# Performance work log

Measured on AMD Instinct MI355X. Metric: run time of the kernel, lower is better.

## Reference

```python
import jax, jax.numpy as jnp
import numpy as np

B, NT, NW, D, H = 32768, 10, 3, 64, 4
EPS = 1e-5

def _ln(x, g, b):
    mu = jnp.mean(x, axis=-1, keepdims=True)
    var = jnp.mean((x - mu) ** 2, axis=-1, keepdims=True)
    return (x - mu) * jax.lax.rsqrt(var + EPS) * g + b

def _mha(q_in, kv, wq, bq, wk, bk, wv, bv, wo, bo):
    Bb, Lq, Dm = q_in.shape
    Lk = kv.shape[1]
    dh = Dm // H
    q = (q_in @ wq + bq).reshape(Bb, Lq, H, dh)
    k = (kv @ wk + bk).reshape(Bb, Lk, H, dh)
    v = (kv @ wv + bv).reshape(Bb, Lk, H, dh)
    s = jnp.einsum('bqhd,bkhd->bhqk', q, k) / np.float32(np.sqrt(dh))
    a = jax.nn.softmax(s, axis=-1)
    o = jnp.einsum('bhqk,bkhd->bqhd', a, v).reshape(Bb, Lq, Dm)
    return o @ wo + bo

def setup_inputs() -> dict:
    key = jax.random.key(0)
    ks = iter(jax.random.split(key, 40))
    def rn(shape, scale=0.05):
        return jax.random.normal(next(ks), shape, dtype=jnp.float32) * scale
    inp = {
        'track_left': jax.random.normal(next(ks), (B, NT, 2), dtype=jnp.float32),
        'track_right': jax.random.normal(next(ks), (B, NT, 2), dtype=jnp.float32),
        'qemb': rn((NW, D), 1.0),
        'ip_w1': rn((2, D // 2)), 'ip_b1': jnp.zeros((D // 2,), jnp.float32),
        'ip_w2': rn((D // 2, D)), 'ip_b2': jnp.zeros((D,), jnp.float32),
    }
    for p in ('a1', 'a2'):
        for nm in ('wq', 'wk', 'wv', 'wo'):
            inp[p + '_' + nm] = rn((D, D))
        for nm in ('bq', 'bk', 'bv', 'bo'):
            inp[p + '_' + nm] = jnp.zeros((D,), jnp.float32)
    inp['ffn_w1'] = rn((D, 2 * D)); inp['ffn_b1'] = jnp.zeros((2 * D,), jnp.float32)
    inp['ffn_w2'] = rn((2 * D, D)); inp['ffn_b2'] = jnp.zeros((D,), jnp.float32)
    for n in ('n1', 'n2', 'n3'):
        inp[n + '_g'] = jnp.ones((D,), jnp.float32)
        inp[n + '_b'] = jnp.zeros((D,), jnp.float32)
    inp['op_w1'] = rn((D, D // 2)); inp['op_b1'] = jnp.zeros((D // 2,), jnp.float32)
    inp['op_w2'] = rn((D // 2, 2)); inp['op_b2'] = jnp.zeros((2,), jnp.float32)
    return inp

def reference(track_left, track_right, qemb, ip_w1, ip_b1, ip_w2, ip_b2,
              a1_wq, a1_bq, a1_wk, a1_bk, a1_wv, a1_bv, a1_wo, a1_bo,
              a2_wq, a2_bq, a2_wk, a2_bk, a2_wv, a2_bv, a2_wo, a2_bo,
              ffn_w1, ffn_b1, ffn_w2, ffn_b2,
              n1_g, n1_b, n2_g, n2_b, n3_g, n3_b,
              op_w1, op_b1, op_w2, op_b2):
    # concat left/right boundaries -> [B, 2*NT, 2]
    pts = jnp.concatenate([track_left, track_right], axis=1)
    # input projection MLP -> [B, 2*NT, D]
    feats = jax.nn.relu(pts @ ip_w1 + ip_b1) @ ip_w2 + ip_b2
    # learned waypoint queries broadcast over batch -> [B, NW, D]
    q0 = jnp.broadcast_to(qemb[None], (pts.shape[0], NW, D))
    x1 = _ln(q0 + _mha(q0, feats, a1_wq, a1_bq, a1_wk, a1_bk, a1_wv, a1_bv, a1_wo, a1_bo), n1_g, n1_b)
    x2 = _ln(x1 + _mha(x1, feats, a2_wq, a2_bq, a2_wk, a2_bk, a2_wv, a2_bv, a2_wo, a2_bo), n2_g, n2_b)
    f = jax.nn.relu(x2 @ ffn_w1 + ffn_b1) @ ffn_w2 + ffn_b2
    x3 = _ln(x2 + f, n3_g, n3_b)
    # output projection -> [B, NW, 2]
    return jax.nn.relu(x3 @ op_w1 + op_b1) @ op_w2 + op_b2
```

## Files before the change

kernel.cpp:

```cpp
#include <hip/hip_runtime.h>
#include <math.h>

#define SCALE 0.36067376022224085f

#define WVF1F 0
#define WVF2F 2048
#define WKT2F 4096
#define G1F   6144
#define BVF1F 6528
#define BVF2F 6592

#define WSYNC() do { asm volatile("s_waitcnt lgkmcnt(0)" ::: "memory"); __builtin_amdgcn_wave_barrier(); } while (0)

struct Params {
  const float* tl; const float* tr; const float* qemb;
  const float* ip_w1; const float* ip_b1;
  const float* wq2; const float* bq2;
  const float* wo1; const float* bo1;
  const float* wo2; const float* bo2;
  const float* ffn_w1; const float* ffn_b1;
  const float* ffn_w2; const float* ffn_b2;
  const float* n1_g; const float* n1_b;
  const float* n2_g; const float* n2_b;
  const float* n3_g; const float* n3_b;
  const float* op_w1; const float* op_b1;
  const float* op_w2; const float* op_b2;
  const float* ws;
  float* out;
};

__global__ void prep1_kernel(const float* ip_w2, const float* ip_b2,
                             const float* wk2, const float* wv1, const float* wv2,
                             const float* bv1, const float* bv2, float* ws) {
  const int bid = blockIdx.x, tid = threadIdx.x;
  if (bid < 24) {
    const int idx = bid * 256 + tid;
    const int mat = idx >> 11;
    const int rem = idx & 2047;
    const int j = rem >> 6, c = rem & 63;
    const float* W = (mat == 0) ? wv1 : (mat == 1) ? wv2 : wk2;
    float acc = 0.f;
    for (int m = 0; m < 64; ++m) acc = fmaf(ip_w2[j * 64 + m], W[m * 64 + c], acc);
    if (mat == 0)      ws[WVF1F + j * 64 + c] = acc;
    else if (mat == 1) ws[WVF2F + j * 64 + c] = acc;
    else               ws[WKT2F + c * 32 + j] = acc * SCALE;
  } else if (tid < 128) {
    const int l = tid >> 6, d = tid & 63;
    const float* bv = l ? bv2 : bv1;
    const float* wv = l ? wv2 : wv1;
    float acc = bv[d];
    for (int m = 0; m < 64; ++m) acc = fmaf(ip_b2[m], wv[m * 64 + d], acc);
    ws[(l ? BVF2F : BVF1F) + d] = acc;
  }
}

__global__ void prep2_kernel(const float* ip_w2, const float* wk1,
                             const float* qemb, const float* wq1, const float* bq1,
                             float* ws) {
  __shared__ float wkf[32][64];
  __shared__ float q1[3][64];
  const int tid = threadIdx.x;
  for (int e = tid; e < 2048; e += 384) {
    const int j = e >> 6, c = e & 63;
    float acc = 0.f;
    for (int m = 0; m < 64; ++m) acc = fmaf(ip_w2[j * 64 + m], wk1[m * 64 + c], acc);
    wkf[j][c] = acc;
  }
  if (tid < 192) {
    const int q = tid >> 6, d = tid & 63;
    float acc = bq1[d];
    for (int e = 0; e < 64; ++e) acc = fmaf(qemb[q * 64 + e], wq1[e * 64 + d], acc);
    q1[q][d] = acc;
  }
  __syncthreads();
  {
    const int r = tid >> 5, j = tid & 31;
    const int h = r / 3, q = r - h * 3;
    float acc = 0.f;
    for (int d = 0; d < 16; ++d) acc = fmaf(wkf[j][h * 16 + d], q1[q][h * 16 + d], acc);
    ws[G1F + r * 32 + j] = acc * SCALE;
  }
}

__global__ __launch_bounds__(256) void planner_kernel(Params p) {
  const int w = threadIdx.x >> 6;
  const int lane = threadIdx.x & 63;
  const int item = blockIdx.x * 4 + w;

  __shared__ __align__(16) float g1_s[12][36];
  __shared__ __align__(16) float a_s[4][20][36];
  __shared__ __align__(16) float att_s[4][12][24];
  __shared__ __align__(16) float ch_s[4][12][36];
  __shared__ __align__(16) float qx_s[4][3][68];
  __shared__ __align__(16) float x_s[4][3][68];
  __shared__ float pts_s[4][40];

  const float* ws = p.ws;

  for (int e = threadIdx.x; e < 384; e += 256)
    g1_s[e >> 5][e & 31] = ws[G1F + e];

  if (lane < 40)
    pts_s[w][lane] = (lane < 20) ? p.tl[item * 20 + lane] : p.tr[item * 20 + lane - 20];
  WSYNC();

  {
    const int j = lane & 31, th = lane >> 5;
    const float w0 = p.ip_w1[j], w1 = p.ip_w1[32 + j], b = p.ip_b1[j];
#pragma unroll
    for (int i = 0; i < 10; ++i) {
      const int t = th * 10 + i;
      a_s[w][t][j] = fmaxf(fmaf(pts_s[w][2 * t], w0, fmaf(pts_s[w][2 * t + 1], w1, b)), 0.f);
    }
  }
  __syncthreads();

  const int t3 = lane / 3;
  const int q3 = lane - t3 * 3;
  const int j32 = lane & 31, half = lane >> 5, hq0 = half * 6;
  const int h16 = lane >> 4;

  float xq[3];

#pragma unroll
  for (int l = 0; l < 2; ++l) {
    if (l == 1) {
      float acc[3];
#pragma unroll
      for (int q = 0; q < 3; ++q) acc[q] = p.bq2[lane];
#pragma unroll
      for (int jc = 0; jc < 16; ++jc) {
        float wv[4];
#pragma unroll
        for (int r = 0; r < 4; ++r) wv[r] = p.wq2[(jc * 4 + r) * 64 + lane];
#pragma unroll
        for (int q = 0; q < 3; ++q) {
          const float4 xv = *(const float4*)&x_s[w][q][jc * 4];
          acc[q] = fmaf(xv.x, wv[0], fmaf(xv.y, wv[1], fmaf(xv.z, wv[2], fmaf(xv.w, wv[3], acc[q]))));
        }
      }
#pragma unroll
      for (int q = 0; q < 3; ++q) qx_s[w][q][lane] = acc[q];
      WSYNC();
      {
        float g2[6] = {0, 0, 0, 0, 0, 0};
        const int D0 = half * 32;
#pragma unroll
        for (int dd = 0; dd < 32; ++dd) {
          const int D = D0 + dd;
          const float wk = ws[WKT2F + D * 32 + j32];
          const int hl = dd >> 4;
#pragma unroll
          for (int q = 0; q < 3; ++q)
            g2[hl * 3 + q] = fmaf(wk, qx_s[w][q][D], g2[hl * 3 + q]);
        }
#pragma unroll
        for (int k = 0; k < 6; ++k) ch_s[w][hq0 + k][j32] = g2[k];
      }
      WSYNC();
    }

    const float (*g)[36] = (l == 0) ? (const float (*)[36])g1_s : (const float (*)[36])ch_s[w];
    if (lane < 60) {
      float acc[4] = {0, 0, 0, 0};
#pragma unroll
      for (int jc = 0; jc < 8; ++jc) {
        const float4 av = *(const float4*)&a_s[w][t3][jc * 4];
#pragma unroll
        for (int h = 0; h < 4; ++h) {
          const float4 gv = *(const float4*)&g[h * 3 + q3][jc * 4];
          acc[h] = fmaf(av.x, gv.x, fmaf(av.y, gv.y, fmaf(av.z, gv.z, fmaf(av.w, gv.w, acc[h]))));
        }
      }
#pragma unroll
      for (int h = 0; h < 4; ++h) att_s[w][h * 3 + q3][t3] = acc[h];
    }
    WSYNC();

    if (lane < 12) {
      float m = -1e30f;
#pragma unroll
      for (int t = 0; t < 20; ++t) m = fmaxf(m, att_s[w][lane][t]);
      float s = 0.f;
#pragma unroll
      for (int t = 0; t < 20; ++t) {
        const float e = exp2f(att_s[w][lane][t] - m);
        att_s[w][lane][t] = e;
        s += e;
      }
      att_s[w][lane][20] = 1.f / s;
    }
    WSYNC();

    {
      float c[6] = {0, 0, 0, 0, 0, 0};
#pragma unroll
      for (int tc = 0; tc < 5; ++tc) {
        float av[4];
#pragma unroll
        for (int r = 0; r < 4; ++r) av[r] = a_s[w][tc * 4 + r][j32];
#pragma unroll
        for (int k = 0; k < 6; ++k) {
          const float4 at = *(const float4*)&att_s[w][hq0 + k][tc * 4];
          c[k] = fmaf(at.x, av[0], fmaf(at.y, av[1], fmaf(at.z, av[2], fmaf(at.w, av[3], c[k]))));
        }
      }
#pragma unroll
      for (int k = 0; k < 6; ++k)
        ch_s[w][hq0 + k][j32] = c[k] * att_s[w][hq0 + k][20];
    }
    WSYNC();

    {
      const float* Wv = ws + (l ? WVF2F : WVF1F);
      const float bv = ws[(l ? BVF2F : BVF1F) + lane];
      float o[3] = {bv, bv, bv};
#pragma unroll
      for (int jc = 0; jc < 8; ++jc) {
        float wv[4];
#pragma unroll
        for (int r = 0; r < 4; ++r) wv[r] = Wv[(jc * 4 + r) * 64 + lane];
#pragma unroll
        for (int q = 0; q < 3; ++q) {
          const float4 cv = *(const float4*)&ch_s[w][h16 * 3 + q][jc * 4];
          o[q] = fmaf(cv.x, wv[0], fmaf(cv.y, wv[1], fmaf(cv.z, wv[2], fmaf(cv.w, wv[3], o[q]))));
        }
      }
#pragma unroll
      for (int q = 0; q < 3; ++q) qx_s[w][q][lane] = o[q];
    }
    WSYNC();

    {
      const float* wo = l ? p.wo2 : p.wo1;
      const float* bo = l ? p.bo2 : p.bo1;
      const float* gg = l ? p.n2_g : p.n1_g;
      const float* gb = l ? p.n2_b : p.n1_b;
      float acc[3];
#pragma unroll
      for (int q = 0; q < 3; ++q)
        acc[q] = bo[lane] + (l ? x_s[w][q][lane] : p.qemb[q * 64 + lane]);
#pragma unroll
      for (int jc = 0; jc < 16; ++jc) {
        float wv[4];
#pragma unroll
        for (int r = 0; r < 4; ++r) wv[r] = wo[(jc * 4 + r) * 64 + lane];
#pragma unroll
        for (int q = 0; q < 3; ++q) {
          const float4 ov = *(const float4*)&qx_s[w][q][jc * 4];
          acc[q] = fmaf(ov.x, wv[0], fmaf(ov.y, wv[1], fmaf(ov.z, wv[2], fmaf(ov.w, wv[3], acc[q]))));
        }
      }
      const float gv = gg[lane], bv = gb[lane];
#pragma unroll
      for (int q = 0; q < 3; ++q) {
        const float v = acc[q];
        float s = v;
#pragma unroll
        for (int m = 32; m >= 1; m >>= 1) s += __shfl_xor(s, m);
        const float mu = s * (1.f / 64.f);
        const float d = v - mu;
        float s2 = d * d;
#pragma unroll
        for (int m = 32; m >= 1; m >>= 1) s2 += __shfl_xor(s2, m);
        const float inv = rsqrtf(s2 * (1.f / 64.f) + 1e-5f);
        const float xn = fmaf(d * inv, gv, bv);
        xq[q] = xn;
        x_s[w][q][lane] = xn;
      }
    }
    WSYNC();
  }

  float* f1p = (float*)a_s[w];
  {
    float a0[3], a1[3];
    const float b0 = p.ffn_b1[lane], b1 = p.ffn_b1[64 + lane];
#pragma unroll
    for (int q = 0; q < 3; ++q) { a0[q] = b0; a1[q] = b1; }
#pragma unroll
    for (int jc = 0; jc < 16; ++jc) {
      float w0[4], w1[4];
#pragma unroll
      for (int r = 0; r < 4; ++r) {
        w0[r] = p.ffn_w1[(jc * 4 + r) * 128 + lane];
        w1[r] = p.ffn_w1[(jc * 4 + r) * 128 + 64 + lane];
      }
#pragma unroll
      for (int q = 0; q < 3; ++q) {
        const float4 xv = *(const float4*)&x_s[w][q][jc * 4];
        a0[q] = fmaf(xv.x, w0[0], fmaf(xv.y, w0[1], fmaf(xv.z, w0[2], fmaf(xv.w, w0[3], a0[q]))));
        a1[q] = fmaf(xv.x, w1[0], fmaf(xv.y, w1[1], fmaf(xv.z, w1[2], fmaf(xv.w, w1[3], a1[q]))));
      }
    }
#pragma unroll
    for (int q = 0; q < 3; ++q) {
      f1p[q * 136 + lane] = fmaxf(a0[q], 0.f);
      f1p[q * 136 + 64 + lane] = fmaxf(a1[q], 0.f);
    }
  }
  WSYNC();

  {
    float acc[3];
#pragma unroll
    for (int q = 0; q < 3; ++q) acc[q] = p.ffn_b2[lane] + xq[q];
#pragma unroll
    for (int mc = 0; mc < 32; ++mc) {
      float wv[4];
#pragma unroll
      for (int r = 0; r < 4; ++r) wv[r] = p.ffn_w2[(mc * 4 + r) * 64 + lane];
#pragma unroll
      for (int q = 0; q < 3; ++q) {
        const float4 fv = *(const float4*)&f1p[q * 136 + mc * 4];
        acc[q] = fmaf(fv.x, wv[0], fmaf(fv.y, wv[1], fmaf(fv.z, wv[2], fmaf(fv.w, wv[3], acc[q]))));
      }
    }
    const float gv = p.n3_g[lane], bv = p.n3_b[lane];
#pragma unroll
    for (int q = 0; q < 3; ++q) {
      const float v = acc[q];
      float s = v;
#pragma unroll
      for (int m = 32; m >= 1; m >>= 1) s += __shfl_xor(s, m);
      const float mu = s * (1.f / 64.f);
      const float d = v - mu;
      float s2 = d * d;
#pragma unroll
      for (int m = 32; m >= 1; m >>= 1) s2 += __shfl_xor(s2, m);
      const float inv = rsqrtf(s2 * (1.f / 64.f) + 1e-5f);
      x_s[w][q][lane] = fmaf(d * inv, gv, bv);
    }
  }
  WSYNC();

  if (lane < 32) {
    float acc[3];
#pragma unroll
    for (int q = 0; q < 3; ++q) acc[q] = p.op_b1[lane];
#pragma unroll
    for (int jc = 0; jc < 16; ++jc) {
      float wv[4];
#pragma unroll
      for (int r = 0; r < 4; ++r) wv[r] = p.op_w1[(jc * 4 + r) * 32 + lane];
#pragma unroll
      for (int q = 0; q < 3; ++q) {
        const float4 xv = *(const float4*)&x_s[w][q][jc * 4];
        acc[q] = fmaf(xv.x, wv[0], fmaf(xv.y, wv[1], fmaf(xv.z, wv[2], fmaf(xv.w, wv[3], acc[q]))));
      }
    }
#pragma unroll
    for (int q = 0; q < 3; ++q) qx_s[w][q][lane] = fmaxf(acc[q], 0.f);
  }
  WSYNC();

  if (lane < 6) {
    const int q = lane >> 1, e = lane & 1;
    float acc = p.op_b2[e];
#pragma unroll
    for (int m = 0; m < 32; ++m) acc = fmaf(qx_s[w][q][m], p.op_w2[m * 2 + e], acc);
    p.out[item * 6 + q * 2 + e] = acc;
  }
}

extern "C" void kernel_launch(void* const* d_in, const int* in_sizes, int n_in,
                              void* d_out, int out_size, void* d_ws, size_t ws_size,
                              hipStream_t stream) {
  const float* in[40];
  for (int i = 0; i < n_in && i < 40; ++i) in[i] = (const float*)d_in[i];

  const float *a1_wq, *a1_wk, *a1_wv, *a1_wo, *a1_bq, *a1_bk, *a1_bv, *a1_bo;
  const float *a2_wq, *a2_wk, *a2_wv, *a2_wo, *a2_bq, *a2_bk, *a2_bv, *a2_bo;
  if (in_sizes[8] == 4096) {
    a1_wq = in[7];  a1_wk = in[8];  a1_wv = in[9];  a1_wo = in[10];
    a1_bq = in[11]; a1_bk = in[12]; a1_bv = in[13]; a1_bo = in[14];
    a2_wq = in[15]; a2_wk = in[16]; a2_wv = in[17]; a2_wo = in[18];
    a2_bq = in[19]; a2_bk = in[20]; a2_bv = in[21]; a2_bo = in[22];
  } else {
    a1_wq = in[7];  a1_bq = in[8];  a1_wk = in[9];  a1_bk = in[10];
    a1_wv = in[11]; a1_bv = in[12]; a1_wo = in[13]; a1_bo = in[14];
    a2_wq = in[15]; a2_bq = in[16]; a2_wk = in[17]; a2_bk = in[18];
    a2_wv = in[19]; a2_bv = in[20]; a2_wo = in[21]; a2_bo = in[22];
  }
  (void)a1_bk; (void)a2_bk;

  float* ws = (float*)d_ws;
  prep1_kernel<<<25, 256, 0, stream>>>(in[5], in[6], a2_wk, a1_wv, a2_wv, a1_bv, a2_bv, ws);
  prep2_kernel<<<1, 384, 0, stream>>>(in[5], a1_wk, in[2], a1_wq, a1_bq, ws);

  Params p;
  p.tl = in[0]; p.tr = in[1]; p.qemb = in[2];
  p.ip_w1 = in[3]; p.ip_b1 = in[4];
  p.wq2 = a2_wq; p.bq2 = a2_bq;
  p.wo1 = a1_wo; p.bo1 = a1_bo;
  p.wo2 = a2_wo; p.bo2 = a2_bo;
  p.ffn_w1 = in[23]; p.ffn_b1 = in[24]; p.ffn_w2 = in[25]; p.ffn_b2 = in[26];
  p.n1_g = in[27]; p.n1_b = in[28]; p.n2_g = in[29]; p.n2_b = in[30];
  p.n3_g = in[31]; p.n3_b = in[32];
  p.op_w1 = in[33]; p.op_b1 = in[34]; p.op_w2 = in[35]; p.op_b2 = in[36];
  p.ws = ws; p.out = (float*)d_out;

  planner_kernel<<<8192, 256, 0, stream>>>(p);
}
```

Baseline: 258.1 us.

## Rewrite planner kernel around split-bf16 MFMA with two items per wave

Replaces the scalar FMA matrix products with 16x16x32 bf16 MFMA instructions, using a three-term hi/lo bf16 split to approximate fp32 accuracy. Weights are pre-split and pre-swizzled into fragment layout by new prep kernels, and each wave now processes two batch items, so the grid is halved. Small parameters are staged in shared memory. The aim is to cut VALU work per item; the cost is extra conversion work, larger LDS use that may reduce occupancy, and a small loss of precision.

```diff
diff --git a/kernel.cpp b/kernel.cpp
--- a/kernel.cpp
+++ b/kernel.cpp
@@ -3,363 +3,571 @@
 
 #define SCALE 0.36067376022224085f
 
-#define WVF1F 0
-#define WVF2F 2048
-#define WKT2F 4096
-#define G1F   6144
-#define BVF1F 6528
-#define BVF2F 6592
+typedef __attribute__((ext_vector_type(8))) short short8;
+typedef __attribute__((ext_vector_type(4))) float f32x4;
+
+#define G1H 0
+#define G1L 512
+#define WV1H 1024
+#define WV1L 3072
+#define WV2H 5120
+#define WV2L 7168
+#define WKT2H 9216
+#define WKT2L 11264
+#define WQ2H 13312
+#define WQ2L 17408
+#define WO1H 21504
+#define WO1L 25600
+#define WO2H 29696
+#define WO2L 33792
+#define F1H 37888
+#define F1L 46080
+#define F2H 54272
+#define F2L 62464
+#define OP1H 70656
+#define OP1L 72704
+#define WKF1T 37376
+#define WKF2T 39424
+#define WVF1T 41472
+#define WVF2T 43520
+#define Q1T   45568
+#define BV1T  45760
 
 #define WSYNC() do { asm volatile("s_waitcnt lgkmcnt(0)" ::: "memory"); __builtin_amdgcn_wave_barrier(); } while (0)
 
+__device__ __forceinline__ unsigned short f2bf(float x) {
+  unsigned u = __builtin_bit_cast(unsigned, x);
+  return (unsigned short)((u + 0x7fffu + ((u >> 16) & 1u)) >> 16);
+}
+__device__ __forceinline__ float bf2f(unsigned short h) {
+  unsigned u = ((unsigned)h) << 16;
+  return __builtin_bit_cast(float, u);
+}
+__device__ __forceinline__ void lds_frag(const float* row, int koff, short8& fh, short8& fl) {
+  const float4 a = *(const float4*)(row + koff);
+  const float4 b = *(const float4*)(row + koff + 4);
+  float v[8] = {a.x, a.y, a.z, a.w, b.x, b.y, b.z, b.w};
+#pragma unroll
+  for (int j = 0; j < 8; ++j) {
+    unsigned short h = f2bf(v[j]);
+    fh[j] = (short)h;
+    fl[j] = (short)f2bf(v[j] - bf2f(h));
+  }
+}
+__device__ __forceinline__ short8 ldg_frag(const unsigned short* base, int idx) {
+  return __builtin_bit_cast(short8, *(const float4*)(base + idx));
+}
+#define MFMA3(acc, ah, al, bh, bl)                                      \
+  acc = __builtin_amdgcn_mfma_f32_16x16x32_bf16(ah, bh, acc, 0, 0, 0);  \
+  acc = __builtin_amdgcn_mfma_f32_16x16x32_bf16(ah, bl, acc, 0, 0, 0);  \
+  acc = __builtin_amdgcn_mfma_f32_16x16x32_bf16(al, bh, acc, 0, 0, 0);
+
 struct Params {
-  const float* tl; const float* tr; const float* qemb;
-  const float* ip_w1; const float* ip_b1;
-  const float* wq2; const float* bq2;
-  const float* wo1; const float* bo1;
-  const float* wo2; const float* bo2;
-  const float* ffn_w1; const float* ffn_b1;
-  const float* ffn_w2; const float* ffn_b2;
-  const float* n1_g; const float* n1_b;
-  const float* n2_g; const float* n2_b;
-  const float* n3_g; const float* n3_b;
-  const float* op_w1; const float* op_b1;
-  const float* op_w2; const float* op_b2;
-  const float* ws;
+  const float *tl, *tr, *qemb, *ip_w1, *ip_b1;
+  const float *bq2, *bo1, *bo2, *fb1, *fb2, *opb1, *opw2, *opb2;
+  const float *n1g, *n1b, *n2g, *n2b, *n3g, *n3b;
+  const float* wsf;
+  const unsigned short* wsb;
   float* out;
 };
 
-__global__ void prep1_kernel(const float* ip_w2, const float* ip_b2,
-                             const float* wk2, const float* wv1, const float* wv2,
-                             const float* bv1, const float* bv2, float* ws) {
+__global__ void prepA_kernel(const float* ip_w2, const float* ip_b2,
+                             const float* wk1, const float* wk2,
+                             const float* wv1, const float* wv2,
+                             const float* bv1, const float* bv2,
+                             const float* qemb, const float* wq1, const float* bq1,
+                             float* wsf) {
   const int bid = blockIdx.x, tid = threadIdx.x;
-  if (bid < 24) {
-    const int idx = bid * 256 + tid;
-    const int mat = idx >> 11;
-    const int rem = idx & 2047;
+  if (bid < 32) {
+    const int e = bid * 256 + tid;
+    const int mat = e >> 11, rem = e & 2047;
     const int j = rem >> 6, c = rem & 63;
-    const float* W = (mat == 0) ? wv1 : (mat == 1) ? wv2 : wk2;
+    const float* W = (mat == 0) ? wk1 : (mat == 1) ? wk2 : (mat == 2) ? wv1 : wv2;
     float acc = 0.f;
     for (int m = 0; m < 64; ++m) acc = fmaf(ip_w2[j * 64 + m], W[m * 64 + c], acc);
-    if (mat == 0)      ws[WVF1F + j * 64 + c] = acc;
-    else if (mat == 1) ws[WVF2F + j * 64 + c] = acc;
-    else               ws[WKT2F + c * 32 + j] = acc * SCALE;
-  } else if (tid < 128) {
-    const int l = tid >> 6, d = tid & 63;
-    const float* bv = l ? bv2 : bv1;
-    const float* wv = l ? wv2 : wv1;
-    float acc = bv[d];
-    for (int m = 0; m < 64; ++m) acc = fmaf(ip_b2[m], wv[m * 64 + d], acc);
-    ws[(l ? BVF2F : BVF1F) + d] = acc;
-  }
-}
-
-__global__ void prep2_kernel(const float* ip_w2, const float* wk1,
-                             const float* qemb, const float* wq1, const float* bq1,
-                             float* ws) {
-  __shared__ float wkf[32][64];
-  __shared__ float q1[3][64];
-  const int tid = threadIdx.x;
-  for (int e = tid; e < 2048; e += 384) {
-    const int j = e >> 6, c = e & 63;
-    float acc = 0.f;
-    for (int m = 0; m < 64; ++m) acc = fmaf(ip_w2[j * 64 + m], wk1[m * 64 + c], acc);
-    wkf[j][c] = acc;
-  }
-  if (tid < 192) {
-    const int q = tid >> 6, d = tid & 63;
-    float acc = bq1[d];
-    for (int e = 0; e < 64; ++e) acc = fmaf(qemb[q * 64 + e], wq1[e * 64 + d], acc);
-    q1[q][d] = acc;
+    wsf[WKF1T + e] = acc;
+  } else if (bid == 32) {
+    if (tid < 192) {
+      const int q = tid >> 6, d = tid & 63;
+      float acc = bq1[d];
+      for (int e = 0; e < 64; ++e) acc = fmaf(qemb[q * 64 + e], wq1[e * 64 + d], acc);
+      wsf[Q1T + tid] = acc;
+    }
+  } else {
+    if (tid < 128) {
+      const int lyr = tid >> 6, d = tid & 63;
+      const float* bv = lyr ? bv2 : bv1;
+      const float* wv = lyr ? wv2 : wv1;
+      float acc = bv[d];
+      for (int m = 0; m < 64; ++m) acc = fmaf(ip_b2[m], wv[m * 64 + d], acc);
+      wsf[BV1T + tid] = acc;
+    }
+  }
+}
+
+__global__ void prepB_kernel(float* wsf, unsigned short* wsb,
+                             const float* wq2, const float* wo1, const float* wo2,
+                             const float* fw1, const float* fw2, const float* opw1) {
+  const int bid = blockIdx.x, tid = threadIdx.x;
+  if (bid == 0) {
+    __shared__ float g1f[32][16];
+    {
+      const int j = tid >> 4, col = tid & 15;
+      float acc = 0.f;
+      if (col < 12) {
+        const int h = (col * 11) >> 5, q = col - 3 * h;
+        for (int d = 0; d < 16; ++d)
+          acc = fmaf(wsf[WKF1T + j * 64 + h * 16 + d], wsf[Q1T + q * 64 + h * 16 + d], acc);
+        acc *= SCALE;
+      }
+      g1f[j][col] = acc;
+    }
+    __syncthreads();
+    {
+      const int e = tid, j8 = e & 7, ln = (e >> 3) & 63;
+      const int k = (ln >> 4) * 8 + j8, n = ln & 15;
+      const float val = g1f[k][n];
+      const unsigned short h = f2bf(val);
+      wsb[G1H + e] = h;
+      wsb[G1L + e] = f2bf(val - bf2f(h));
+    }
+    return;
+  }
+  const int pe = (bid - 1) * 512 + tid;
+  const int j8 = pe & 7, ln = (pe >> 3) & 63;
+  const int krow = (ln >> 4) * 8 + j8, ncol = ln & 15;
+  float val;
+  int hOff, lOff, loc;
+  if (pe < 2048) {
+    loc = pe; const int nt = (loc >> 9) & 3;
+    val = wsf[WVF1T + krow * 64 + nt * 16 + ncol];
+    hOff = WV1H; lOff = WV1L;
+  } else if (pe < 4096) {
+    loc = pe - 2048; const int nt = (loc >> 9) & 3;
+    val = wsf[WVF2T + krow * 64 + nt * 16 + ncol];
+    hOff = WV2H; lOff = WV2L;
+  } else if (pe < 6144) {
+    loc = pe - 4096; const int nt = (loc >> 9) & 1, kt = (loc >> 10) & 1;
+    val = SCALE * wsf[WKF2T + (nt * 16 + ncol) * 64 + kt * 32 + krow];
+    hOff = WKT2H; lOff = WKT2L;
+  } else if (pe < 10240) {
+    loc = pe - 6144; const int nt = (loc >> 9) & 3, kt = (loc >> 11) & 1;
+    val = wq2[(kt * 32 + krow) * 64 + nt * 16 + ncol];
+    hOff = WQ2H; lOff = WQ2L;
+  } else if (pe < 14336) {
+    loc = pe - 10240; const int nt = (loc >> 9) & 3, kt = (loc >> 11) & 1;
+    val = wo1[(kt * 32 + krow) * 64 + nt * 16 + ncol];
+    hOff = WO1H; lOff = WO1L;
+  } else if (pe < 18432) {
+    loc = pe - 14336; const int nt = (loc >> 9) & 3, kt = (loc >> 11) & 1;
+    val = wo2[(kt * 32 + krow) * 64 + nt * 16 + ncol];
+    hOff = WO2H; lOff = WO2L;
+  } else if (pe < 26624) {
+    loc = pe - 18432; const int nt = (loc >> 9) & 7, kt = (loc >> 12) & 1;
+    val = fw1[(kt * 32 + krow) * 128 + nt * 16 + ncol];
+    hOff = F1H; lOff = F1L;
+  } else if (pe < 34816) {
+    loc = pe - 26624; const int nt = (loc >> 9) & 3, kt = (loc >> 11) & 3;
+    val = fw2[(kt * 32 + krow) * 64 + nt * 16 + ncol];
+    hOff = F2H; lOff = F2L;
+  } else {
+    loc = pe - 34816; const int nt = (loc >> 9) & 1, kt = (loc >> 10) & 1;
+    val = opw1[(kt * 32 + krow) * 32 + nt * 16 + ncol];
+    hOff = OP1H; lOff = OP1L;
+  }
+  const unsigned short h = f2bf(val);
+  wsb[hOff + loc] = h;
+  wsb[lOff + loc] = f2bf(val - bf2f(h));
+}
+
+__device__ __forceinline__ void ln_write(float v[4][4], const float* gam, const float* bet,
+                                         float xs[][68], float xq[4][4], int l15, int l4) {
+  float g4[4], b4[4];
+#pragma unroll
+  for (int nt = 0; nt < 4; ++nt) { g4[nt] = gam[nt * 16 + l15]; b4[nt] = bet[nt * 16 + l15]; }
+#pragma unroll
+  for (int reg = 0; reg < 4; ++reg) {
+    float s = v[0][reg] + v[1][reg] + v[2][reg] + v[3][reg];
+    s += __shfl_xor(s, 1); s += __shfl_xor(s, 2); s += __shfl_xor(s, 4); s += __shfl_xor(s, 8);
+    const float mu = s * 0.015625f;
+    float d[4];
+#pragma unroll
+    for (int nt = 0; nt < 4; ++nt) d[nt] = v[nt][reg] - mu;
+    float s2 = d[0]*d[0] + d[1]*d[1] + d[2]*d[2] + d[3]*d[3];
+    s2 += __shfl_xor(s2, 1); s2 += __shfl_xor(s2, 2); s2 += __shfl_xor(s2, 4); s2 += __shfl_xor(s2, 8);
+    const float inv = rsqrtf(fmaf(s2, 0.015625f, 1e-5f));
+    const int r = l4 * 4 + reg;
+#pragma unroll
+    for (int nt = 0; nt < 4; ++nt) {
+      const float xn = fmaf(d[nt] * inv, g4[nt], b4[nt]);
+      xq[nt][reg] = xn;
+      if (r < 6) xs[r][nt * 16 + l15] = xn;
+    }
+  }
+}
+
+__global__ __launch_bounds__(256) void planner_kernel(Params p) {
+  const int w = threadIdx.x >> 6, l = threadIdx.x & 63;
+  const int l15 = l & 15, l4 = l >> 4;
+  const unsigned short* wb = p.wsb;
+
+  __shared__ __align__(16) float a_s[4][64][36];
+  __shared__ __align__(16) float att_s[4][2][12][24];
+  __shared__ __align__(16) float g2_s[4][2][12][36];
+  __shared__ __align__(16) float x_s[4][6][68];
+  __shared__ __align__(16) float o_s[4][6][68];
+  __shared__ float pts_s[4][2][40];
+  __shared__ float qemb_s[192];
+  __shared__ float nrm_s[6][64];
+  __shared__ float bias4_s[4][64];
+  __shared__ float fb1_s[128];
+  __shared__ float opb1_s[32];
+  __shared__ float opw2_s[64];
+  __shared__ float opb2_s[2];
+  __shared__ float bvf_s[2][64];
+  __shared__ float ipw_s[2][32];
+  __shared__ float ipb_s[32];
+
+  {
+    const int t = threadIdx.x;
+    if (t < 192) qemb_s[t] = p.qemb[t];
+    for (int e = t; e < 384; e += 256) {
+      const int k = e >> 6, d = e & 63;
+      float v = (k == 0) ? p.n1g[d] : (k == 1) ? p.n1b[d] : (k == 2) ? p.n2g[d]
+              : (k == 3) ? p.n2b[d] : (k == 4) ? p.n3g[d] : p.n3b[d];
+      nrm_s[k][d] = v;
+    }
+    {
+      const int k = t >> 6, d = t & 63;
+      bias4_s[k][d] = (k == 0) ? p.bo1[d] : (k == 1) ? p.bo2[d] : (k == 2) ? p.bq2[d] : p.fb2[d];
+    }
+    if (t < 128) fb1_s[t] = p.fb1[t];
+    if (t < 32) opb1_s[t] = p.opb1[t];
+    if (t < 64) opw2_s[t] = p.opw2[t];
+    if (t < 2) opb2_s[t] = p.opb2[t];
+    if (t < 128) bvf_s[t >> 6][t & 63] = p.wsf[BV1T + t];
+    if (t < 64) ipw_s[t >> 5][t & 31] = p.ip_w1[t];
+    if (t < 32) ipb_s[t] = p.ip_b1[t];
   }
   __syncthreads();
+
+  float (*aw)[36] = a_s[w];
+  const int itemBase = blockIdx.x * 8 + w * 2;
+
+#pragma unroll
+  for (int pass = 0; pass < 2; ++pass) {
+    const int idx = pass * 64 + l;
+    if (idx < 80) {
+      const int i = idx / 40, r = idx - 40 * i;
+      pts_s[w][i][r] = (r < 20) ? p.tl[(itemBase + i) * 20 + r] : p.tr[(itemBase + i) * 20 + r - 20];
+    }
+  }
+  WSYNC();
   {
-    const int r = tid >> 5, j = tid & 31;
-    const int h = r / 3, q = r - h * 3;
-    float acc = 0.f;
-    for (int d = 0; d < 16; ++d) acc = fmaf(wkf[j][h * 16 + d], q1[q][h * 16 + d], acc);
-    ws[G1F + r * 32 + j] = acc * SCALE;
-  }
-}
-
-__global__ __launch_bounds__(256) void planner_kernel(Params p) {
-  const int w = threadIdx.x >> 6;
-  const int lane = threadIdx.x & 63;
-  const int item = blockIdx.x * 4 + w;
-
-  __shared__ __align__(16) float g1_s[12][36];
-  __shared__ __align__(16) float a_s[4][20][36];
-  __shared__ __align__(16) float att_s[4][12][24];
-  __shared__ __align__(16) float ch_s[4][12][36];
-  __shared__ __align__(16) float qx_s[4][3][68];
-  __shared__ __align__(16) float x_s[4][3][68];
-  __shared__ float pts_s[4][40];
-
-  const float* ws = p.ws;
-
-  for (int e = threadIdx.x; e < 384; e += 256)
-    g1_s[e >> 5][e & 31] = ws[G1F + e];
-
-  if (lane < 40)
-    pts_s[w][lane] = (lane < 20) ? p.tl[item * 20 + lane] : p.tr[item * 20 + lane - 20];
+    const int i = l >> 5, j = l & 31;
+    const float w0 = ipw_s[0][j], w1 = ipw_s[1][j], b = ipb_s[j];
+#pragma unroll
+    for (int tt = 0; tt < 20; ++tt) {
+      const float h = fmaf(pts_s[w][i][2 * tt], w0, fmaf(pts_s[w][i][2 * tt + 1], w1, b));
+      aw[i * 32 + tt][j] = fmaxf(h, 0.f);
+    }
+#pragma unroll
+    for (int tt = 20; tt < 32; ++tt) aw[i * 32 + tt][j] = 0.f;
+  }
+  for (int e = l; e < 96; e += 64) {
+    const int i = e / 48, rem = e - 48 * i;
+    att_s[w][i][rem >> 2][20 + (rem & 3)] = 0.f;
+  }
   WSYNC();
 
-  {
-    const int j = lane & 31, th = lane >> 5;
-    const float w0 = p.ip_w1[j], w1 = p.ip_w1[32 + j], b = p.ip_b1[j];
-#pragma unroll
-    for (int i = 0; i < 10; ++i) {
-      const int t = th * 10 + i;
-      a_s[w][t][j] = fmaxf(fmaf(pts_s[w][2 * t], w0, fmaf(pts_s[w][2 * t + 1], w1, b)), 0.f);
-    }
-  }
-  __syncthreads();
-
-  const int t3 = lane / 3;
-  const int q3 = lane - t3 * 3;
-  const int j32 = lane & 31, half = lane >> 5, hq0 = half * 6;
-  const int h16 = lane >> 4;
-
-  float xq[3];
-
-#pragma unroll
-  for (int l = 0; l < 2; ++l) {
-    if (l == 1) {
-      float acc[3];
-#pragma unroll
-      for (int q = 0; q < 3; ++q) acc[q] = p.bq2[lane];
-#pragma unroll
-      for (int jc = 0; jc < 16; ++jc) {
-        float wv[4];
-#pragma unroll
-        for (int r = 0; r < 4; ++r) wv[r] = p.wq2[(jc * 4 + r) * 64 + lane];
-#pragma unroll
-        for (int q = 0; q < 3; ++q) {
-          const float4 xv = *(const float4*)&x_s[w][q][jc * 4];
-          acc[q] = fmaf(xv.x, wv[0], fmaf(xv.y, wv[1], fmaf(xv.z, wv[2], fmaf(xv.w, wv[3], acc[q]))));
+  float xq1[4][4], xq2[4][4], xq3[4][4];
+
+#pragma unroll 1
+  for (int lyr = 0; lyr < 2; ++lyr) {
+    {
+      f32x4 S[4];
+      short8 bh, bl;
+      if (lyr == 0) { bh = ldg_frag(wb + G1H, l * 8); bl = ldg_frag(wb + G1L, l * 8); }
+#pragma unroll
+      for (int mt = 0; mt < 4; ++mt) {
+        if (lyr == 1 && (mt & 1) == 0)
+          lds_frag(&g2_s[w][mt >> 1][min(l15, 11)][0], l4 * 8, bh, bl);
+        short8 ah, al;
+        lds_frag(&aw[mt * 16 + l15][0], l4 * 8, ah, al);
+        S[mt] = (f32x4){0.f, 0.f, 0.f, 0.f};
+        MFMA3(S[mt], ah, al, bh, bl);
+      }
+#pragma unroll
+      for (int i = 0; i < 2; ++i) {
+        float sv[8];
+        float m = -3.0e38f;
+#pragma unroll
+        for (int mo = 0; mo < 2; ++mo)
+#pragma unroll
+          for (int r = 0; r < 4; ++r) {
+            float s = S[i * 2 + mo][r];
+            if (mo == 1 && l4 != 0) s = -3.0e38f;
+            sv[mo * 4 + r] = s;
+            m = fmaxf(m, s);
+          }
+        m = fmaxf(m, __shfl_xor(m, 16)); m = fmaxf(m, __shfl_xor(m, 32));
+        float sum = 0.f;
+#pragma unroll
+        for (int k = 0; k < 8; ++k) { sv[k] = exp2f(sv[k] - m); sum += sv[k]; }
+        sum += __shfl_xor(sum, 16); sum += __shfl_xor(sum, 32);
+        const float inv = 1.f / sum;
+#pragma unroll
+        for (int mo = 0; mo < 2; ++mo)
+#pragma unroll
+          for (int r = 0; r < 4; ++r) {
+            const int tt = mo * 16 + l4 * 4 + r;
+            if (l15 < 12 && tt < 20) att_s[w][i][l15][tt] = sv[mo * 4 + r] * inv;
+          }
+      }
+    }
+    WSYNC();
+
+    {
+      const int vh = lyr ? WV2H : WV1H, vl = lyr ? WV2L : WV1L;
+      float op[2][3][4];
+#pragma unroll
+      for (int i = 0; i < 2; ++i)
+#pragma unroll
+        for (int q = 0; q < 3; ++q)
+#pragma unroll
+          for (int nt = 0; nt < 4; ++nt) op[i][q][nt] = 0.f;
+#pragma unroll
+      for (int mt = 0; mt < 4; ++mt) {
+        short8 ah, al;
+        lds_frag(&aw[mt * 16 + l15][0], l4 * 8, ah, al);
+        const int i = mt >> 1;
+        const int tb = min((mt & 1) * 16 + l4 * 4, 20);
+#pragma unroll
+        for (int nt = 0; nt < 4; ++nt) {
+          short8 bh = ldg_frag(wb + vh, (nt * 64 + l) * 8);
+          short8 bl = ldg_frag(wb + vl, (nt * 64 + l) * 8);
+          f32x4 acc = (f32x4){0.f, 0.f, 0.f, 0.f};
+          MFMA3(acc, ah, al, bh, bl);
+#pragma unroll
+          for (int q = 0; q < 3; ++q) {
+            const float4 av = *(const float4*)&att_s[w][i][nt * 3 + q][tb];
+            op[i][q][nt] = fmaf(av.x, acc[0], op[i][q][nt]);
+            op[i][q][nt] = fmaf(av.y, acc[1], op[i][q][nt]);
+            op[i][q][nt] = fmaf(av.z, acc[2], op[i][q][nt]);
+            op[i][q][nt] = fmaf(av.w, acc[3], op[i][q][nt]);
+          }
         }
       }
 #pragma unroll
-      for (int q = 0; q < 3; ++q) qx_s[w][q][lane] = acc[q];
+      for (int i = 0; i < 2; ++i)
+#pragma unroll
+        for (int q = 0; q < 3; ++q)
+#pragma unroll
+          for (int nt = 0; nt < 4; ++nt) {
+            float v = op[i][q][nt];
+            v += __shfl_xor(v, 16); v += __shfl_xor(v, 32);
+            if (l4 == 0) o_s[w][i * 3 + q][nt * 16 + l15] = v + bvf_s[lyr][nt * 16 + l15];
+          }
+    }
+    WSYNC();
+
+    {
+      const int oh = lyr ? WO2H : WO1H, ol = lyr ? WO2L : WO1L;
+      f32x4 acc[4];
+#pragma unroll
+      for (int nt = 0; nt < 4; ++nt) acc[nt] = (f32x4){0.f, 0.f, 0.f, 0.f};
+#pragma unroll
+      for (int kt = 0; kt < 2; ++kt) {
+        short8 ah, al;
+        lds_frag(&o_s[w][min(l15, 5)][0], kt * 32 + l4 * 8, ah, al);
+#pragma unroll
+        for (int nt = 0; nt < 4; ++nt) {
+          short8 bh = ldg_frag(wb + oh, ((kt * 4 + nt) * 64 + l) * 8);
+          short8 bl = ldg_frag(wb + ol, ((kt * 4 + nt) * 64 + l) * 8);
+          MFMA3(acc[nt], ah, al, bh, bl);
+        }
+      }
+      float v[4][4];
+#pragma unroll
+      for (int nt = 0; nt < 4; ++nt)
+#pragma unroll
+        for (int reg = 0; reg < 4; ++reg) {
+          const int r = l4 * 4 + reg, rr = min(r, 5);
+          const int d = nt * 16 + l15;
+          float resid;
+          if (lyr == 0) {
+            const int qq = rr - 3 * (rr >= 3);
+            resid = qemb_s[qq * 64 + d];
+          } else {
+            resid = xq1[nt][reg];
+          }
+          v[nt][reg] = acc[nt][reg] + bias4_s[lyr][d] + resid;
+        }
+      ln_write(v, nrm_s[lyr * 2], nrm_s[lyr * 2 + 1], x_s[w],
+               (lyr == 0) ? xq1 : xq2, l15, l4);
+    }
+    WSYNC();
+
+    if (lyr == 0) {
+      {
+        f32x4 acc[4];
+#pragma unroll
+        for (int nt = 0; nt < 4; ++nt) acc[nt] = (f32x4){0.f, 0.f, 0.f, 0.f};
+#pragma unroll
+        for (int kt = 0; kt < 2; ++kt) {
+          short8 ah, al;
+          lds_frag(&x_s[w][min(l15, 5)][0], kt * 32 + l4 * 8, ah, al);
+#pragma unroll
+          for (int nt = 0; nt < 4; ++nt) {
+            short8 bh = ldg_frag(wb + WQ2H, ((kt * 4 + nt) * 64 + l) * 8);
+            short8 bl = ldg_frag(wb + WQ2L, ((kt * 4 + nt) * 64 + l) * 8);
+            MFMA3(acc[nt], ah, al, bh, bl);
+          }
+        }
+#pragma unroll
+        for (int nt = 0; nt < 4; ++nt)
+#pragma unroll
+          for (int reg = 0; reg < 4; ++reg) {
+            const int r = l4 * 4 + reg;
+            if (r < 6) o_s[w][r][nt * 16 + l15] = acc[nt][reg] + bias4_s[2][nt * 16 + l15];
+          }
+      }
       WSYNC();
       {
-        float g2[6] = {0, 0, 0, 0, 0, 0};
-        const int D0 = half * 32;
-#pragma unroll
-        for (int dd = 0; dd < 32; ++dd) {
-          const int D = D0 + dd;
-          const float wk = ws[WKT2F + D * 32 + j32];
-          const int hl = dd >> 4;
-#pragma unroll
-          for (int q = 0; q < 3; ++q)
-            g2[hl * 3 + q] = fmaf(wk, qx_s[w][q][D], g2[hl * 3 + q]);
+        f32x4 ga[2][2];
+#pragma unroll
+        for (int mt = 0; mt < 2; ++mt)
+#pragma unroll
+          for (int nt = 0; nt < 2; ++nt) ga[mt][nt] = (f32x4){0.f, 0.f, 0.f, 0.f};
+#pragma unroll
+        for (int mt = 0; mt < 2; ++mt) {
+          const int arow = min(mt * 16 + l15, 23);
+          const int ia = arow >= 12;
+          const int hqa = arow - 12 * ia;
+          const int h = (hqa * 11) >> 5;
+          const int qa = hqa - 3 * h;
+          const float* qrow = &o_s[w][ia * 3 + qa][0];
+#pragma unroll
+          for (int kt = 0; kt < 2; ++kt) {
+            short8 ah, al;
+            lds_frag(qrow, kt * 32 + l4 * 8, ah, al);
+            const bool match = (kt * 2 + (l4 >> 1)) == h;
+            if (!match) {
+              const short8 z = {0, 0, 0, 0, 0, 0, 0, 0};
+              ah = z; al = z;
+            }
+#pragma unroll
+            for (int nt = 0; nt < 2; ++nt) {
+              short8 bh = ldg_frag(wb + WKT2H, ((kt * 2 + nt) * 64 + l) * 8);
+              short8 bl = ldg_frag(wb + WKT2L, ((kt * 2 + nt) * 64 + l) * 8);
+              MFMA3(ga[mt][nt], ah, al, bh, bl);
+            }
+          }
         }
 #pragma unroll
-        for (int k = 0; k < 6; ++k) ch_s[w][hq0 + k][j32] = g2[k];
+        for (int mt = 0; mt < 2; ++mt)
+#pragma unroll
+          for (int nt = 0; nt < 2; ++nt)
+#pragma unroll
+            for (int reg = 0; reg < 4; ++reg) {
+              const int row = mt * 16 + l4 * 4 + reg;
+              if (row < 24) {
+                const int ia = row >= 12;
+                g2_s[w][ia][row - 12 * ia][nt * 16 + l15] = ga[mt][nt][reg];
+              }
+            }
       }
       WSYNC();
     }
-
-    const float (*g)[36] = (l == 0) ? (const float (*)[36])g1_s : (const float (*)[36])ch_s[w];
-    if (lane < 60) {
-      float acc[4] = {0, 0, 0, 0};
-#pragma unroll
-      for (int jc = 0; jc < 8; ++jc) {
-        const float4 av = *(const float4*)&a_s[w][t3][jc * 4];
-#pragma unroll
-        for (int h = 0; h < 4; ++h) {
-          const float4 gv = *(const float4*)&g[h * 3 + q3][jc * 4];
-          acc[h] = fmaf(av.x, gv.x, fmaf(av.y, gv.y, fmaf(av.z, gv.z, fmaf(av.w, gv.w, acc[h]))));
+  }
+
+  float* fbuf = (float*)a_s[w];
+  {
+    f32x4 acc[8];
+#pragma unroll
+    for (int nt = 0; nt < 8; ++nt) acc[nt] = (f32x4){0.f, 0.f, 0.f, 0.f};
+#pragma unroll
+    for (int kt = 0; kt < 2; ++kt) {
+      short8 ah, al;
+      lds_frag(&x_s[w][min(l15, 5)][0], kt * 32 + l4 * 8, ah, al);
+#pragma unroll
+      for (int nt = 0; nt < 8; ++nt) {
+        short8 bh = ldg_frag(wb + F1H, ((kt * 8 + nt) * 64 + l) * 8);
+        short8 bl = ldg_frag(wb + F1L, ((kt * 8 + nt) * 64 + l) * 8);
+        MFMA3(acc[nt], ah, al, bh, bl);
+      }
+    }
+#pragma unroll
+    for (int nt = 0; nt < 8; ++nt)
+#pragma unroll
+      for (int reg = 0; reg < 4; ++reg) {
+        const int r = l4 * 4 + reg;
+        if (r < 6) {
+          const int d = nt * 16 + l15;
+          fbuf[r * 132 + d] = fmaxf(acc[nt][reg] + fb1_s[d], 0.f);
         }
       }
-#pragma unroll
-      for (int h = 0; h < 4; ++h) att_s[w][h * 3 + q3][t3] = acc[h];
-    }
-    WSYNC();
-
-    if (lane < 12) {
-      float m = -1e30f;
-#pragma unroll
-      for (int t = 0; t < 20; ++t) m = fmaxf(m, att_s[w][lane][t]);
-      float s = 0.f;
-#pragma unroll
-      for (int t = 0; t < 20; ++t) {
-        const float e = exp2f(att_s[w][lane][t] - m);
-        att_s[w][lane][t] = e;
-        s += e;
-      }
-      att_s[w][lane][20] = 1.f / s;
-    }
-    WSYNC();
-
-    {
-      float c[6] = {0, 0, 0, 0, 0, 0};
-#pragma unroll
-      for (int tc = 0; tc < 5; ++tc) {
-        float av[4];
-#pragma unroll
-        for (int r = 0; r < 4; ++r) av[r] = a_s[w][tc * 4 + r][j32];
-#pragma unroll
-        for (int k = 0; k < 6; ++k) {
-          const float4 at = *(const float4*)&att_s[w][hq0 + k][tc * 4];
-          c[k] = fmaf(at.x, av[0], fmaf(at.y, av[1], fmaf(at.z, av[2], fmaf(at.w, av[3], c[k]))));
-        }
-      }
-#pragma unroll
-      for (int k = 0; k < 6; ++k)
-        ch_s[w][hq0 + k][j32] = c[k] * att_s[w][hq0 + k][20];
-    }
-    WSYNC();
-
-    {
-      const float* Wv = ws + (l ? WVF2F : WVF1F);
-      const float bv = ws[(l ? BVF2F : BVF1F) + lane];
-      float o[3] = {bv, bv, bv};
-#pragma unroll
-      for (int jc = 0; jc < 8; ++jc) {
-        float wv[4];
-#pragma unroll
-        for (int r = 0; r < 4; ++r) wv[r] = Wv[(jc * 4 + r) * 64 + lane];
-#pragma unroll
-        for (int q = 0; q < 3; ++q) {
-          const float4 cv = *(const float4*)&ch_s[w][h16 * 3 + q][jc * 4];
-          o[q] = fmaf(cv.x, wv[0], fmaf(cv.y, wv[1], fmaf(cv.z, wv[2], fmaf(cv.w, wv[3], o[q]))));
-        }
-      }
-#pragma unroll
-      for (int q = 0; q < 3; ++q) qx_s[w][q][lane] = o[q];
-    }
-    WSYNC();
-
-    {
-      const float* wo = l ? p.wo2 : p.wo1;
-      const float* bo = l ? p.bo2 : p.bo1;
-      const float* gg = l ? p.n2_g : p.n1_g;
-      const float* gb = l ? p.n2_b : p.n1_b;
-      float acc[3];
-#pragma unroll
-      for (int q = 0; q < 3; ++q)
-        acc[q] = bo[lane] + (l ? x_s[w][q][lane] : p.qemb[q * 64 + lane]);
-#pragma unroll
-      for (int jc = 0; jc < 16; ++jc) {
-        float wv[4];
-#pragma unroll
-        for (int r = 0; r < 4; ++r) wv[r] = wo[(jc * 4 + r) * 64 + lane];
-#pragma unroll
-        for (int q = 0; q < 3; ++q) {
-          const float4 ov = *(const float4*)&qx_s[w][q][jc * 4];
-          acc[q] = fmaf(ov.x, wv[0], fmaf(ov.y, wv[1], fmaf(ov.z, wv[2], fmaf(ov.w, wv[3], acc[q]))));
-        }
-      }
-      const float gv = gg[lane], bv = gb[lane];
-#pragma unroll
-      for (int q = 0; q < 3; ++q) {
-        const float v = acc[q];
-        float s = v;
-#pragma unroll
-        for (int m = 32; m >= 1; m >>= 1) s += __shfl_xor(s, m);
-        const float mu = s * (1.f / 64.f);
-        const float d = v - mu;
-        float s2 = d * d;
-#pragma unroll
-        for (int m = 32; m >= 1; m >>= 1) s2 += __shfl_xor(s2, m);
-        const float inv = rsqrtf(s2 * (1.f / 64.f) + 1e-5f);
-        const float xn = fmaf(d * inv, gv, bv);
-        xq[q] = xn;
-        x_s[w][q][lane] = xn;
-      }
-    }
-    WSYNC();
-  }
-
-  float* f1p = (float*)a_s[w];
+  }
+  WSYNC();
+
   {
-    float a0[3], a1[3];
-    const float b0 = p.ffn_b1[lane], b1 = p.ffn_b1[64 + lane];
-#pragma unroll
-    for (int q = 0; q < 3; ++q) { a0[q] = b0; a1[q] = b1; }
-#pragma unroll
-    for (int jc = 0; jc < 16; ++jc) {
-      float w0[4], w1[4];
-#pragma unroll
-      for (int r = 0; r < 4; ++r) {
-        w0[r] = p.ffn_w1[(jc * 4 + r) * 128 + lane];
-        w1[r] = p.ffn_w1[(jc * 4 + r) * 128 + 64 + lane];
-      }
-#pragma unroll
-      for (int q = 0; q < 3; ++q) {
-        const float4 xv = *(const float4*)&x_s[w][q][jc * 4];
-        a0[q] = fmaf(xv.x, w0[0], fmaf(xv.y, w0[1], fmaf(xv.z, w0[2], fmaf(xv.w, w0[3], a0[q]))));
-        a1[q] = fmaf(xv.x, w1[0], fmaf(xv.y, w1[1], fmaf(xv.z, w1[2], fmaf(xv.w, w1[3], a1[q]))));
-      }
-    }
-#pragma unroll
-    for (int q = 0; q < 3; ++q) {
-      f1p[q * 136 + lane] = fmaxf(a0[q], 0.f);
-      f1p[q * 136 + 64 + lane] = fmaxf(a1[q], 0.f);
-    }
+    f32x4 acc[4];
+#pragma unroll
+    for (int nt = 0; nt < 4; ++nt) acc[nt] = (f32x4){0.f, 0.f, 0.f, 0.f};
+#pragma unroll
+    for (int kt = 0; kt < 4; ++kt) {
+      short8 ah, al;
+      lds_frag(&fbuf[min(l15, 5) * 132], kt * 32 + l4 * 8, ah, al);
+#pragma unroll
+      for (int nt = 0; nt < 4; ++nt) {
+        short8 bh = ldg_frag(wb + F2H, ((kt * 4 + nt) * 64 + l) * 8);
+        short8 bl = ldg_frag(wb + F2L, ((kt * 4 + nt) * 64 + l) * 8);
+        MFMA3(acc[nt], ah, al, bh, bl);
+      }
+    }
+    float v[4][4];
+#pragma unroll
+    for (int nt = 0; nt < 4; ++nt)
+#pragma unroll
+      for (int reg = 0; reg < 4; ++reg)
+        v[nt][reg] = acc[nt][reg] + bias4_s[3][nt * 16 + l15] + xq2[nt][reg];
+    ln_write(v, nrm_s[4], nrm_s[5], x_s[w], xq3, l15, l4);
+    (void)xq3;
   }
   WSYNC();
 
   {
-    float acc[3];
-#pragma unroll
-    for (int q = 0; q < 3; ++q) acc[q] = p.ffn_b2[lane] + xq[q];
-#pragma unroll
-    for (int mc = 0; mc < 32; ++mc) {
-      float wv[4];
-#pragma unroll
-      for (int r = 0; r < 4; ++r) wv[r] = p.ffn_w2[(mc * 4 + r) * 64 + lane];
-#pragma unroll
-      for (int q = 0; q < 3; ++q) {
-        const float4 fv = *(const float4*)&f1p[q * 136 + mc * 4];
-        acc[q] = fmaf(fv.x, wv[0], fmaf(fv.y, wv[1], fmaf(fv.z, wv[2], fmaf(fv.w, wv[3], acc[q]))));
-      }
-    }
-    const float gv = p.n3_g[lane], bv = p.n3_b[lane];
-#pragma unroll
-    for (int q = 0; q < 3; ++q) {
-      const float v = acc[q];
-      float s = v;
-#pragma unroll
-      for (int m = 32; m >= 1; m >>= 1) s += __shfl_xor(s, m);
-      const float mu = s * (1.f / 64.f);
-      const float d = v - mu;
-      float s2 = d * d;
-#pragma unroll
-      for (int m = 32; m >= 1; m >>= 1) s2 += __shfl_xor(s2, m);
-      const float inv = rsqrtf(s2 * (1.f / 64.f) + 1e-5f);
-      x_s[w][q][lane] = fmaf(d * inv, gv, bv);
-    }
+    f32x4 acc[2];
+#pragma unroll
+    for (int nt = 0; nt < 2; ++nt) acc[nt] = (f32x4){0.f, 0.f, 0.f, 0.f};
+#pragma unroll
+    for (int kt = 0; kt < 2; ++kt) {
+      short8 ah, al;
+      lds_frag(&x_s[w][min(l15, 5)][0], kt * 32 + l4 * 8, ah, al);
+#pragma unroll
+      for (int nt = 0; nt < 2; ++nt) {
+        short8 bh = ldg_frag(wb + OP1H, ((kt * 2 + nt) * 64 + l) * 8);
+        short8 bl = ldg_frag(wb + OP1L, ((kt * 2 + nt) * 64 + l) * 8);
+        MFMA3(acc[nt], ah, al, bh, bl);
+      }
+    }
+#pragma unroll
+    for (int nt = 0; nt < 2; ++nt)
+#pragma unroll
+      for (int reg = 0; reg < 4; ++reg) {
+        const int r = l4 * 4 + reg;
+        if (r < 6) o_s[w][r][nt * 16 + l15] = fmaxf(acc[nt][reg] + opb1_s[nt * 16 + l15], 0.f);
+      }
   }
   WSYNC();
 
-  if (lane < 32) {
-    float acc[3];
-#pragma unroll
-    for (int q = 0; q < 3; ++q) acc[q] = p.op_b1[lane];
-#pragma unroll
-    for (int jc = 0; jc < 16; ++jc) {
-      float wv[4];
-#pragma unroll
-      for (int r = 0; r < 4; ++r) wv[r] = p.op_w1[(jc * 4 + r) * 32 + lane];
-#pragma unroll
-      for (int q = 0; q < 3; ++q) {
-        const float4 xv = *(const float4*)&x_s[w][q][jc * 4];
-        acc[q] = fmaf(xv.x, wv[0], fmaf(xv.y, wv[1], fmaf(xv.z, wv[2], fmaf(xv.w, wv[3], acc[q]))));
-      }
-    }
-#pragma unroll
-    for (int q = 0; q < 3; ++q) qx_s[w][q][lane] = fmaxf(acc[q], 0.f);
-  }
-  WSYNC();
-
-  if (lane < 6) {
-    const int q = lane >> 1, e = lane & 1;
-    float acc = p.op_b2[e];
-#pragma unroll
-    for (int m = 0; m < 32; ++m) acc = fmaf(qx_s[w][q][m], p.op_w2[m * 2 + e], acc);
-    p.out[item * 6 + q * 2 + e] = acc;
+  if (l < 12) {
+    const int r = l >> 1, e = l & 1;
+    float acc = opb2_s[e];
+#pragma unroll
+    for (int m = 0; m < 32; ++m) acc = fmaf(o_s[w][r][m], opw2_s[m * 2 + e], acc);
+    const int i = r >= 3, q = r - 3 * i;
+    p.out[(itemBase + i) * 6 + q * 2 + e] = acc;
   }
 }
 
@@ -384,21 +592,24 @@
   }
   (void)a1_bk; (void)a2_bk;
 
-  float* ws = (float*)d_ws;
-  prep1_kernel<<<25, 256, 0, stream>>>(in[5], in[6], a2_wk, a1_wv, a2_wv, a1_bv, a2_bv, ws);
-  prep2_kernel<<<1, 384, 0, stream>>>(in[5], a1_wk, in[2], a1_wq, a1_bq, ws);
+  float* wsf = (float*)d_ws;
+  unsigned short* wsb = (unsigned short*)d_ws;
+
+  prepA_kernel<<<34, 256, 0, stream>>>(in[5], in[6], a1_wk, a2_wk, a1_wv, a2_wv,
+                                       a1_bv, a2_bv, in[2], a1_wq, a1_bq, wsf);
+  prepB_kernel<<<73, 512, 0, stream>>>(wsf, wsb, a2_wq, a1_wo, a2_wo,
+                                       in[23], in[25], in[33]);
 
   Params p;
   p.tl = in[0]; p.tr = in[1]; p.qemb = in[2];
   p.ip_w1 = in[3]; p.ip_b1 = in[4];
-  p.wq2 = a2_wq; p.bq2 = a2_bq;
-  p.wo1 = a1_wo; p.bo1 = a1_bo;
-  p.wo2 = a2_wo; p.bo2 = a2_bo;
-  p.ffn_w1 = in[23]; p.ffn_b1 = in[24]; p.ffn_w2 = in[25]; p.ffn_b2 = in[26];
-  p.n1_g = in[27]; p.n1_b = in[28]; p.n2_g = in[29]; p.n2_b = in[30];
-  p.n3_g = in[31]; p.n3_b = in[32];
-  p.op_w1 = in[33]; p.op_b1 = in[34]; p.op_w2 = in[35]; p.op_b2 = in[36];
-  p.ws = ws; p.out = (float*)d_out;
-
-  planner_kernel<<<8192, 256, 0, stream>>>(p);
-}
+  p.bq2 = a2_bq; p.bo1 = a1_bo; p.bo2 = a2_bo;
+  p.fb1 = in[24]; p.fb2 = in[26];
+  p.opb1 = in[34]; p.opw2 = in[35]; p.opb2 = in[36];
+  p.n1g = in[27]; p.n1b = in[28]; p.n2g = in[29]; p.n2b = in[30];
+  p.n3g = in[31]; p.n3b = in[32];
+  p.wsf = wsf; p.wsb = wsb;
+  p.out = (float*)d_out;
+
+  planner_kernel<<<4096, 256, 0, stream>>>(p);
+}
```

Result: slower. 469.7 us (+82.0%).
